# Performance work log

Hardware: AMD Instinct MI355X
Metric: run time of the kernel (lower is better)

Reference implementation:

```python
import jax, jax.numpy as jnp
import numpy as np

B, S, H = 4, 2048, 1024  # batch, seq, hidden


def setup_inputs() -> dict:
    key = jax.random.key(0)
    kq, kk, kv = jax.random.split(key, 3)
    return {
        "Q": jax.random.normal(kq, (B, S, H), dtype=jnp.float32),
        "K": jax.random.normal(kk, (B, S, H), dtype=jnp.float32),
        "V": jax.random.normal(kv, (B, S, H), dtype=jnp.float32),
    }


def reference(Q, K, V):
    # Phase of rfft along hidden dim -> [B, S, F], F = H//2 + 1
    q_fft = jnp.fft.rfft(Q, axis=-1)
    k_fft = jnp.fft.rfft(K, axis=-1)
    q_phase = jnp.arctan2(q_fft.imag, q_fft.real)
    k_phase = jnp.arctan2(k_fft.imag, k_fft.real)
    n_freqs = q_phase.shape[-1]
    # mean_f cos(qp_i - kp_j) = (cos(qp) @ cos(kp)^T + sin(qp) @ sin(kp)^T) / F
    # Avoids materializing the [B,S,S,F] phase_diff tensor; math is identical.
    align = (
        jnp.einsum("bif,bjf->bij", jnp.cos(q_phase), jnp.cos(k_phase))
        + jnp.einsum("bif,bjf->bij", jnp.sin(q_phase), jnp.sin(k_phase))
    ) / n_freqs
    scores = align + 1.0
    weights = jax.nn.softmax(scores, axis=-1)  # [B, S, S]
    output = jnp.einsum("bij,bjh->bih", weights, V)  # [B, S, H]
    return output, weights
```

## Files before the change

kernel.cpp:

```cpp
#include <hip/hip_runtime.h>
#include <hip/hip_bf16.h>
#include <math.h>

#define Bb 4
#define Ss 2048
#define Hh 1024
#define Ff 513
#define FEAT 1026
#define KP2 1088

typedef __attribute__((ext_vector_type(8))) short bf16x8;
typedef __attribute__((ext_vector_type(4))) float f32x4;
typedef __attribute__((ext_vector_type(16))) float f32x16;

typedef const __attribute__((address_space(1))) void GVoid;
typedef __attribute__((address_space(3))) void LVoid;

#define PADI(i) ((i) + ((i) >> 4))

__device__ __forceinline__ float2 cmul(float2 a, float2 b) {
  return make_float2(a.x * b.x - a.y * b.y, a.x * b.y + a.y * b.x);
}

__device__ __forceinline__ unsigned short bf16bits(float x) {
  __hip_bfloat16 h = __float2bfloat16(x);
  return *reinterpret_cast<unsigned short*>(&h);
}

__device__ __forceinline__ bf16x8 lds_read_b128(const short* p) {
  bf16x8 r;
  asm volatile("ds_read_b128 %0, %1"
               : "=&v"(r)
               : "v"((const __attribute__((address_space(3))) short*)p));
  return r;
}

__global__ __launch_bounds__(256) void fft_phase_kernel(
    const float* __restrict__ Q, const float* __restrict__ Kin,
    __hip_bfloat16* __restrict__ FQ, __hip_bfloat16* __restrict__ FK) {
  const int row = blockIdx.x;
  const float* qs = Q   + (size_t)row * Hh;
  const float* ks = Kin + (size_t)row * Hh;
  __hip_bfloat16* fq = FQ + (size_t)row * KP2;
  __hip_bfloat16* fk = FK + (size_t)row * KP2;

  __shared__ float2 data[PADI(1023) + 1];
  __shared__ float2 tw[1024];
  const int tid = threadIdx.x;

#pragma unroll
  for (int e = 0; e < 4; ++e) {
    const int m = tid + e * 256;
    float s, c;
    sincosf(-6.283185307179586f * (float)m * (1.0f / 1024.0f), &s, &c);
    tw[m] = make_float2(c, s);
  }
#pragma unroll
  for (int e = 0; e < 4; ++e) {
    const int n = tid + e * 256;
    const int r4 = ((n & 3) << 8) | (((n >> 2) & 3) << 6) | (((n >> 4) & 3) << 4)
                 | (((n >> 6) & 3) << 2) | ((n >> 8) & 3);
    data[PADI(r4)] = make_float2(qs[n], ks[n]);
  }
  __syncthreads();

  int quarter = 1, step = 256;
  for (int s = 0; s < 5; ++s) {
    const int j = tid & (quarter - 1);
    const int pos = 4 * tid - 3 * j;
    const float2 x0 = data[PADI(pos)];
    const float2 x1 = data[PADI(pos + quarter)];
    const float2 x2 = data[PADI(pos + 2 * quarter)];
    const float2 x3 = data[PADI(pos + 3 * quarter)];
    const int e1 = j * step;
    const float2 a1 = cmul(x1, tw[e1]);
    const float2 a2 = cmul(x2, tw[2 * e1]);
    const float2 a3 = cmul(x3, tw[3 * e1]);
    const float2 t0 = make_float2(x0.x + a2.x, x0.y + a2.y);
    const float2 t1 = make_float2(x0.x - a2.x, x0.y - a2.y);
    const float2 t2 = make_float2(a1.x + a3.x, a1.y + a3.y);
    const float2 t3 = make_float2(a1.x - a3.x, a1.y - a3.y);
    data[PADI(pos)]               = make_float2(t0.x + t2.x, t0.y + t2.y);
    data[PADI(pos + quarter)]     = make_float2(t1.x + t3.y, t1.y - t3.x);
    data[PADI(pos + 2 * quarter)] = make_float2(t0.x - t2.x, t0.y - t2.y);
    data[PADI(pos + 3 * quarter)] = make_float2(t1.x - t3.y, t1.y + t3.x);
    __syncthreads();
    quarter <<= 2; step >>= 2;
  }

  for (int f = tid; f <= 512; f += 256) {
    const float2 z1 = data[PADI(f)];
    const float2 z2 = data[PADI((1024 - f) & 1023)];
    const float qr = z1.x + z2.x, qi = z1.y - z2.y;
    const float kr = z1.y + z2.y, ki = z2.x - z1.x;
    float qc, qsn, kc, ksn;
    const float qm2 = qr * qr + qi * qi;
    if (qm2 > 1e-30f) { const float iv = rsqrtf(qm2); qc = qr * iv; qsn = qi * iv; }
    else              { qc = 1.0f; qsn = 0.0f; }
    const float km2 = kr * kr + ki * ki;
    if (km2 > 1e-30f) { const float iv = rsqrtf(km2); kc = kr * iv; ksn = ki * iv; }
    else              { kc = 1.0f; ksn = 0.0f; }
    fq[f] = __float2bfloat16(qc); fq[Ff + f] = __float2bfloat16(qsn);
    fk[f] = __float2bfloat16(kc); fk[Ff + f] = __float2bfloat16(ksn);
  }
  for (int p = FEAT + tid; p < KP2; p += 256) {
    fq[p] = __float2bfloat16(0.0f);
    fk[p] = __float2bfloat16(0.0f);
  }
}

__global__ __launch_bounds__(256) void vt_kernel(
    const float* __restrict__ V, __hip_bfloat16* __restrict__ Vt) {
  const int b = blockIdx.z;
  const int h0 = blockIdx.x * 32;
  const int s0 = blockIdx.y * 32;
  __shared__ float t[32][33];
  const int tid = threadIdx.x;
  const int c = tid & 31;
  const int r8 = tid >> 5;
  const float* Vb = V + (size_t)b * Ss * Hh;
#pragma unroll
  for (int e = 0; e < 4; ++e) {
    const int r = r8 + e * 8;
    t[r][c] = Vb[(size_t)(s0 + r) * Hh + h0 + c];
  }
  __syncthreads();
  __hip_bfloat16* O = Vt + (size_t)b * Hh * Ss;
#pragma unroll
  for (int e = 0; e < 4; ++e) {
    const int hh = r8 + e * 8;
    O[(size_t)(h0 + hh) * Ss + s0 + c] = __float2bfloat16(t[c][hh]);
  }
}

template<int K, int LDA, int LDB, int LDC, int EPI, int BMT>
__global__ __launch_bounds__(512, 2) void gemm32(
    const __hip_bfloat16* __restrict__ Ag, const __hip_bfloat16* __restrict__ Bg,
    float* __restrict__ Cg, size_t strA, size_t strB, size_t strC) {
  constexpr int nt  = K / 64;
  constexpr int MF  = BMT / 64;
  constexpr int MPH = MF / 2;
  constexpr int SAW = MPH;

  const int gx = gridDim.x, gy = gridDim.y;
  const int nwg = gx * gy * (int)gridDim.z;
  int f = ((int)blockIdx.z * gy + (int)blockIdx.y) * gx + (int)blockIdx.x;
  f = (f & 7) * (nwg >> 3) + (f >> 3);
  const int bx = f % gx; f /= gx;
  const int by = f % gy;
  const int bz = f / gy;

  const int i0 = by * BMT;
  const int j0 = bx * 256;
  const char* Ab = (const char*)(Ag + (size_t)bz * strA);
  const char* Bp = (const char*)(Bg + (size_t)bz * strB);
  float* C = Cg + (size_t)bz * strC;

  __shared__ short As[2][BMT * 64];
  __shared__ short Bs[2][256 * 64];

  const int tid = threadIdx.x;
  const int lane = tid & 63;
  const int w  = tid >> 6;
  const int wm = w >> 2;
  const int wn = w & 3;

  f32x16 acc[MF][2];
#pragma unroll
  for (int mi = 0; mi < MF; ++mi)
#pragma unroll
    for (int ni = 0; ni < 2; ++ni)
#pragma unroll
      for (int r = 0; r < 16; ++r) acc[mi][ni][r] = 0.0f;

#define BAR() __builtin_amdgcn_s_barrier()

#define SA(dd, tt, kh)                                                                   \
  do {                                                                                   \
    _Pragma("unroll")                                                                    \
    for (int ii = 0; ii < SAW; ++ii) {                                                   \
      const int f_ = w * SAW + ii;                                                       \
      const int rg_ = f_ >> 1;                                                           \
      const int kc_ = 2 * (kh) + (f_ & 1);                                               \
      __builtin_amdgcn_global_load_lds(                                                  \
          (GVoid*)(Ab + (size_t)(i0 + rg_ * 32 + (lane & 31)) * (LDA * 2) +              \
                   (size_t)(tt) * 128 + kc_ * 32 + (lane >> 5) * 16),                    \
          (LVoid*)&As[dd][(rg_ * 4 + kc_) * 512], 16, 0, 0);                             \
    }                                                                                    \
  } while (0)
#define SB(dd, tt, kh)                                                                   \
  do {                                                                                   \
    _Pragma("unroll")                                                                    \
    for (int ii = 0; ii < 2; ++ii) {                                                     \
      const int f_ = w * 2 + ii;                                                         \
      const int rg_ = f_ >> 1;                                                           \
      const int kc_ = 2 * (kh) + (f_ & 1);                                               \
      __builtin_amdgcn_global_lo\
ad_lds(                                                                                  \
          (GVoid*)(Bp + (size_t)(j0 + rg_ * 32 + (lane & 31)) * (LDB * 2) +              \
                   (size_t)(tt) * 128 + kc_ * 32 + (lane >> 5) * 16),                    \
          (LVoid*)&Bs[dd][(rg_ * 4 + kc_) * 512], 16, 0, 0);                             \
    }                                                                                    \
  } while (0)
#define RA(dd, mh, kh)                                                                   \
  _Pragma("unroll")                                                                      \
  for (int mi = 0; mi < MPH; ++mi)                                                       \
    _Pragma("unroll")                                                                    \
    for (int kb = 0; kb < 2; ++kb)                                                       \
      af[mi][kb] = lds_read_b128(                                                        \
          &As[dd][((wm * MF + (mh) * MPH + mi) * 4 + 2 * (kh) + kb) * 512 + lane * 8]);
#define RB(dd, kh)                                                                       \
  _Pragma("unroll")                                                                      \
  for (int ni = 0; ni < 2; ++ni)                                                         \
    _Pragma("unroll")                                                                    \
    for (int kb = 0; kb < 2; ++kb)                                                       \
      bf[ni][kb] = lds_read_b128(                                                        \
          &Bs[dd][((wn * 2 + ni) * 4 + 2 * (kh) + kb) * 512 + lane * 8]);
#define MM(mh)                                                                           \
  asm volatile("s_waitcnt lgkmcnt(0)");                                                  \
  __builtin_amdgcn_sched_barrier(0);                                                     \
  __builtin_amdgcn_s_setprio(1);                                                         \
  _Pragma("unroll")                                                                      \
  for (int mi = 0; mi < MPH; ++mi)                                                       \
    _Pragma("unroll")                                                                    \
    for (int ni = 0; ni < 2; ++ni)                                                       \
      _Pragma("unroll")                                                                  \
      for (int kb = 0; kb < 2; ++kb)                                                     \
        acc[(mh) * MPH + mi][ni] = __builtin_amdgcn_mfma_f32_32x32x16_bf16(              \
            af[mi][kb], bf[ni][kb], acc[(mh) * MPH + mi][ni], 0, 0, 0);                  \
  __builtin_amdgcn_s_setprio(0);                                                         \
  __builtin_amdgcn_sched_barrier(0);

  SA(0, 0, 0); SA(0, 0, 1); SB(0, 0, 0); SB(0, 0, 1);
  SA(1, 1, 0); SA(1, 1, 1); SB(1, 1, 0); SB(1, 1, 1);
  if constexpr (SAW == 2) asm volatile("s_waitcnt vmcnt(8)");
  else                    asm volatile("s_waitcnt vmcnt(6)");
  BAR();

  for (int t = 0; t < nt; ++t) {
    const int d = t & 1;
    bf16x8 af[MPH][2], bf[2][2];

    RA(d, 0, 0); RB(d, 0);
    if (t >= 1 && t + 1 < nt) SA(d ^ 1, t + 1, 1);
    BAR();
    MM(0);
    BAR();

    RA(d, 1, 0);
    if (t + 2 < nt) SB(d, t + 2, 0);
    BAR();
    MM(1);
    BAR();

    RA(d, 0, 1); RB(d, 1);
    if (t + 2 < nt) SA(d, t + 2, 0);
    BAR();
    MM(0);
    BAR();

    RA(d, 1, 1);
    if (t + 2 < nt) SB(d, t + 2, 1);
    BAR();
    MM(1);
    if (t + 2 < nt) {
      if constexpr (SAW == 2) asm volatile("s_waitcnt vmcnt(6)");
      else                    asm volatile("s_waitcnt vmcnt(5)");
    } else {
      asm volatile("s_waitcnt vmcnt(0)");
    }
    BAR();
  }
#undef SA
#undef SB
#undef RA
#undef RB
#undef MM
#undef BAR

  const int col = lane & 31;
  const int rbase = (lane >> 5) * 4;
#pragma unroll
  for (int mi = 0; mi < MF; ++mi) {
#pragma unroll
    for (int ni = 0; ni < 2; ++ni) {
#pragma unroll
      for (int r = 0; r < 16; ++r) {
        const int row = (r & 3) + 8 * (r >> 2) + rbase;
        const int i = i0 + wm * (MF * 32) + mi * 32 + row;
        const int j = j0 + wn * 64 + ni * 32 + col;
        float v = acc[mi][ni][r];
        if (EPI == 0) v *= (1.0f / 513.0f);
        C[(size_t)i * LDC + j] = v;
      }
    }
  }
}

__global__ __launch_bounds__(256) void softmax_kernel(
    float* __restrict__ W, __hip_bfloat16* __restrict__ Wb) {
  const size_t row = blockIdx.x;
  float* p = W + row * (size_t)Ss;
  __hip_bfloat16* pb = Wb + row * (size_t)Ss;
  const int tid = threadIdx.x;
  __shared__ float red[4];

  const float4* p4 = (const float4*)p;
  const float4 a = p4[2 * tid];
  const float4 bq = p4[2 * tid + 1];
  float v[8] = {a.x, a.y, a.z, a.w, bq.x, bq.y, bq.z, bq.w};

  float m = v[0];
#pragma unroll
  for (int e = 1; e < 8; ++e) m = fmaxf(m, v[e]);
#pragma unroll
  for (int off = 32; off > 0; off >>= 1) m = fmaxf(m, __shfl_xor(m, off, 64));
  if ((tid & 63) == 0) red[tid >> 6] = m;
  __syncthreads();
  m = fmaxf(fmaxf(red[0], red[1]), fmaxf(red[2], red[3]));

  float sum = 0.0f;
#pragma unroll
  for (int e = 0; e < 8; ++e) { v[e] = __expf(v[e] - m); sum += v[e]; }
#pragma unroll
  for (int off = 32; off > 0; off >>= 1) sum += __shfl_xor(sum, off, 64);
  __syncthreads();
  if ((tid & 63) == 0) red[tid >> 6] = sum;
  __syncthreads();
  sum = red[0] + red[1] + red[2] + red[3];

  const float rs = 1.0f / sum;
#pragma unroll
  for (int e = 0; e < 8; ++e) v[e] *= rs;

  float4* o4 = (float4*)p;
  o4[2 * tid]     = make_float4(v[0], v[1], v[2], v[3]);
  o4[2 * tid + 1] = make_float4(v[4], v[5], v[6], v[7]);

  bf16x8 ob;
#pragma unroll
  for (int e = 0; e < 8; ++e) ob[e] = (short)bf16bits(v[e]);
  *(bf16x8*)&pb[8 * tid] = ob;
}

extern "C" void kernel_launch(void* const* d_in, const int* in_sizes, int n_in,
                              void* d_out, int out_size, void* d_ws, size_t ws_size,
                              hipStream_t stream) {
  const float* Q = (const float*)d_in[0];
  const float* K = (const float*)d_in[1];
  const float* V = (const float*)d_in[2];

  float* out     = (float*)d_out;
  float* weights = out + (size_t)Bb * Ss * Hh;

  __hip_bfloat16* FQb = (__hip_bfloat16*)d_ws;
  __hip_bfloat16* FKb = FQb + (size_t)Bb * Ss * KP2;
  __hip_bfloat16* Vtb = FKb + (size_t)Bb * Ss * KP2;
  __hip_bfloat16* Wb  = (__hip_bfloat16*)d_ws;

  hipLaunchKernelGGL(fft_phase_kernel, dim3(Bb * Ss), dim3(256), 0, stream,
                     Q, K, FQb, FKb);
  hipLaunchKernelGGL(vt_kernel, dim3(Hh / 32, Ss / 32, Bb), dim3(256), 0, stream,
                     V, Vtb);
  hipLaunchKernelGGL((gemm32<KP2, KP2, KP2, Ss, 0, 256>), dim3(Ss / 256, Ss / 256, Bb),
                     dim3(512), 0, stream, FQb, FKb, weights,
                     (size_t)Ss * KP2, (size_t)Ss * KP2, (size_t)Ss * Ss);
  hipLaunchKernelGGL(softmax_kernel, dim3(Bb * Ss), dim3(256), 0, stream,
                     weights, Wb);
  hipLaunchKernelGGL((gemm32<Ss, Ss, Ss, Hh, 1, 128>), dim3(Hh / 256, Ss / 128, Bb),
                     dim3(512), 0, stream, Wb, Vtb, out,
                     (size_t)Ss * Ss, (size_t)Hh * Ss, (size_t)Ss * Hh);
}
```

Measured before the change: 169.3 us.

## Restructure GEMM main loop into two k-half phases with fewer barriers

Replaces the four-phase per-tile schedule (split over M halves and K halves) with two phases over K halves, each loading all M fragments and issuing all MFMAs at once. Global-to-LDS prefetches for the next tiles are regrouped and the vmcnt wait counts are adjusted to match. The intent is to cut the number of workgroup barriers and lgkmcnt waits per tile. In exchange it needs more live A-fragment registers per phase and changes how well memory loads overlap with compute.

```diff
diff --git a/kernel.cpp b/kernel.cpp
--- a/kernel.cpp
+++ b/kernel.cpp
@@ -139,8 +139,7 @@
     float* __restrict__ Cg, size_t strA, size_t strB, size_t strC) {
   constexpr int nt  = K / 64;
   constexpr int MF  = BMT / 64;
-  constexpr int MPH = MF / 2;
-  constexpr int SAW = MPH;
+  constexpr int SAW = BMT / 128;
 
   const int gx = gridDim.x, gy = gridDim.y;
   const int nwg = gx * gy * (int)gridDim.z;
@@ -195,20 +194,19 @@
       const int f_ = w * 2 + ii;                                                         \
       const int rg_ = f_ >> 1;                                                           \
       const int kc_ = 2 * (kh) + (f_ & 1);                                               \
-      __builtin_amdgcn_global_lo\
-ad_lds(                                                                                  \
+      __builtin_amdgcn_global_load_lds(                                                  \
           (GVoid*)(Bp + (size_t)(j0 + rg_ * 32 + (lane & 31)) * (LDB * 2) +              \
                    (size_t)(tt) * 128 + kc_ * 32 + (lane >> 5) * 16),                    \
           (LVoid*)&Bs[dd][(rg_ * 4 + kc_) * 512], 16, 0, 0);                             \
     }                                                                                    \
   } while (0)
-#define RA(dd, mh, kh)                                                                   \
+#define RA(dd, kh)                                                                       \
   _Pragma("unroll")                                                                      \
-  for (int mi = 0; mi < MPH; ++mi)                                                       \
+  for (int mi = 0; mi < MF; ++mi)                                                        \
     _Pragma("unroll")                                                                    \
     for (int kb = 0; kb < 2; ++kb)                                                       \
       af[mi][kb] = lds_read_b128(                                                        \
-          &As[dd][((wm * MF + (mh) * MPH + mi) * 4 + 2 * (kh) + kb) * 512 + lane * 8]);
+          &As[dd][((wm * MF + mi) * 4 + 2 * (kh) + kb) * 512 + lane * 8]);
 #define RB(dd, kh)                                                                       \
   _Pragma("unroll")                                                                      \
   for (int ni = 0; ni < 2; ++ni)                                                         \
@@ -216,56 +214,42 @@
     for (int kb = 0; kb < 2; ++kb)                                                       \
       bf[ni][kb] = lds_read_b128(                                                        \
           &Bs[dd][((wn * 2 + ni) * 4 + 2 * (kh) + kb) * 512 + lane * 8]);
-#define MM(mh)                                                                           \
+#define MM()                                                                             \
   asm volatile("s_waitcnt lgkmcnt(0)");                                                  \
   __builtin_amdgcn_sched_barrier(0);                                                     \
   __builtin_amdgcn_s_setprio(1);                                                         \
   _Pragma("unroll")                                                                      \
-  for (int mi = 0; mi < MPH; ++mi)                                                       \
+  for (int mi = 0; mi < MF; ++mi)                                                        \
     _Pragma("unroll")                                                                    \
     for (int ni = 0; ni < 2; ++ni)                                                       \
       _Pragma("unroll")                                                                  \
       for (int kb = 0; kb < 2; ++kb)                                                     \
-        acc[(mh) * MPH + mi][ni] = __builtin_amdgcn_mfma_f32_32x32x16_bf16(              \
-            af[mi][kb], bf[ni][kb], acc[(mh) * MPH + mi][ni], 0, 0, 0);                  \
+        acc[mi][ni] = __builtin_amdgcn_mfma_f32_32x32x16_bf16(                           \
+            af[mi][kb], bf[ni][kb], acc[mi][ni], 0, 0, 0);                               \
   __builtin_amdgcn_s_setprio(0);                                                         \
   __builtin_amdgcn_sched_barrier(0);
 
-  SA(0, 0, 0); SA(0, 0, 1); SB(0, 0, 0); SB(0, 0, 1);
-  SA(1, 1, 0); SA(1, 1, 1); SB(1, 1, 0); SB(1, 1, 1);
-  if constexpr (SAW == 2) asm volatile("s_waitcnt vmcnt(8)");
-  else                    asm volatile("s_waitcnt vmcnt(6)");
+  SA(0, 0, 0); SB(0, 0, 0); SA(0, 0, 1); SB(0, 0, 1);
+  SA(1, 1, 0); SB(1, 1, 0);
+  if constexpr (SAW == 2) asm volatile("s_waitcnt vmcnt(4)");
+  else                    asm volatile("s_waitcnt vmcnt(3)");
   BAR();
 
   for (int t = 0; t < nt; ++t) {
     const int d = t & 1;
-    bf16x8 af[MPH][2], bf[2][2];
-
-    RA(d, 0, 0); RB(d, 0);
-    if (t >= 1 && t + 1 < nt) SA(d ^ 1, t + 1, 1);
+    bf16x8 af[MF][2], bf[2][2];
+
+    RA(d, 0); RB(d, 0);
+    if (t + 1 < nt) { SA(d ^ 1, t + 1, 1); SB(d ^ 1, t + 1, 1); }
+    MM();
     BAR();
-    MM(0);
-    BAR();
-
-    RA(d, 1, 0);
-    if (t + 2 < nt) SB(d, t + 2, 0);
-    BAR();
-    MM(1);
-    BAR();
-
-    RA(d, 0, 1); RB(d, 1);
-    if (t + 2 < nt) SA(d, t + 2, 0);
-    BAR();
-    MM(0);
-    BAR();
-
-    RA(d, 1, 1);
-    if (t + 2 < nt) SB(d, t + 2, 1);
-    BAR();
-    MM(1);
+
+    RA(d, 1); RB(d, 1);
+    if (t + 2 < nt) { SA(d, t + 2, 0); SB(d, t + 2, 0); }
+    MM();
     if (t + 2 < nt) {
-      if constexpr (SAW == 2) asm volatile("s_waitcnt vmcnt(6)");
-      else                    asm volatile("s_waitcnt vmcnt(5)");
+      if constexpr (SAW == 2) asm volatile("s_waitcnt vmcnt(4)");
+      else                    asm volatile("s_waitcnt vmcnt(3)");
     } else {
       asm volatile("s_waitcnt vmcnt(0)");
     }
```

After: 169.3 us. No clear change (+0.0%).
